# Kernel optimization log

Measured on AMD Instinct MI355X. Metric: run time of the kernel, lower is better.

The kernel has to match this reference:

```python
import jax, jax.numpy as jnp
import numpy as np

B, N = 4096, 2048


def setup_inputs() -> dict:
    key = jax.random.key(0)
    k1, k2, k3, k4 = jax.random.split(key, 4)
    return {
        "src_pts3d": jax.random.normal(k1, (B, N, 3), dtype=jnp.float32),
        "tgt_pts3d": jax.random.normal(k2, (B, N, 3), dtype=jnp.float32),
        "kpt_src_mask": jax.random.uniform(k3, (B, N), dtype=jnp.float32),
        "kpt_tgt_mask": jax.random.uniform(k4, (B, N), dtype=jnp.float32),
    }


def reference(src_pts3d, tgt_pts3d, kpt_src_mask, kpt_tgt_mask):
    # H = src^T @ diag(mask_tgt) @ tgt, fused as a masked row-scale contraction: [B,3,3]
    H = jnp.einsum('bnc,bn,bnd->bcd', src_pts3d, kpt_tgt_mask, tgt_pts3d)
    # torch.svd returns V (H = U S V^T); jnp returns Vh, so V = Vh^T
    u, s, vh = jnp.linalg.svd(H)
    v = jnp.swapaxes(vh, -1, -2)              # [B,3,3]
    ut = jnp.swapaxes(u, -1, -2)              # [B,3,3]
    r = v @ ut
    det = jnp.linalg.det(r)                   # [B]
    # branch-free reflection fix: negate 3rd column of V when det(r) < 0
    sign = jnp.where(det < 0, -1.0, 1.0)
    col_scale = jnp.stack([jnp.ones_like(sign), jnp.ones_like(sign), sign], axis=-1)  # [B,3]
    R = (v * col_scale[:, None, :]) @ ut
    return R
```

## Files before the change

kernel.cpp:

```cpp
#include <hip/hip_runtime.h>
#include <math.h>

#define BATCH 4096
#define NPTS  2048
#define THREADS 256

typedef float f32x4 __attribute__((ext_vector_type(4)));

__device__ __forceinline__ f32x4 ntload(const f32x4* p) {
    return __builtin_nontemporal_load(p);
}

#define ACC(sx, sy, sz, tx, ty, tz, mm) do {                                   \
    float d0 = (mm) * (tx), d1 = (mm) * (ty), d2 = (mm) * (tz);                \
    h[0] = fmaf((sx), d0, h[0]); h[1] = fmaf((sx), d1, h[1]); h[2] = fmaf((sx), d2, h[2]); \
    h[3] = fmaf((sy), d0, h[3]); h[4] = fmaf((sy), d1, h[4]); h[5] = fmaf((sy), d2, h[5]); \
    h[6] = fmaf((sz), d0, h[6]); h[7] = fmaf((sz), d1, h[7]); h[8] = fmaf((sz), d2, h[8]); \
} while (0)

__global__ __launch_bounds__(THREADS, 4)
void reduce_kernel(const float* __restrict__ src, const float* __restrict__ tgt,
                   const float* __restrict__ mask, float* __restrict__ Hout)
{
    const int b   = blockIdx.x;
    const int t   = threadIdx.x;
    const f32x4* s4 = (const f32x4*)(src  + (size_t)b * (NPTS * 3));
    const f32x4* t4 = (const f32x4*)(tgt  + (size_t)b * (NPTS * 3));
    const f32x4* m4 = (const f32x4*)(mask + (size_t)b * NPTS);

    f32x4 m0  = ntload(&m4[t]);
    f32x4 m1  = ntload(&m4[t + 256]);
    f32x4 sa0 = ntload(&s4[3 * t + 0]);
    f32x4 sb0 = ntload(&s4[3 * t + 1]);
    f32x4 sc0 = ntload(&s4[3 * t + 2]);
    f32x4 ta0 = ntload(&t4[3 * t + 0]);
    f32x4 tb0 = ntload(&t4[3 * t + 1]);
    f32x4 tc0 = ntload(&t4[3 * t + 2]);
    f32x4 sa1 = ntload(&s4[3 * (t + 256) + 0]);
    f32x4 sb1 = ntload(&s4[3 * (t + 256) + 1]);
    f32x4 sc1 = ntload(&s4[3 * (t + 256) + 2]);
    f32x4 ta1 = ntload(&t4[3 * (t + 256) + 0]);
    f32x4 tb1 = ntload(&t4[3 * (t + 256) + 1]);
    f32x4 tc1 = ntload(&t4[3 * (t + 256) + 2]);

    float h[9] = {0.f, 0.f, 0.f, 0.f, 0.f, 0.f, 0.f, 0.f, 0.f};
    ACC(sa0.x, sa0.y, sa0.z, ta0.x, ta0.y, ta0.z, m0.x);
    ACC(sa0.w, sb0.x, sb0.y, ta0.w, tb0.x, tb0.y, m0.y);
    ACC(sb0.z, sb0.w, sc0.x, tb0.z, tb0.w, tc0.x, m0.z);
    ACC(sc0.y, sc0.z, sc0.w, tc0.y, tc0.z, tc0.w, m0.w);
    ACC(sa1.x, sa1.y, sa1.z, ta1.x, ta1.y, ta1.z, m1.x);
    ACC(sa1.w, sb1.x, sb1.y, ta1.w, tb1.x, tb1.y, m1.y);
    ACC(sb1.z, sb1.w, sc1.x, tb1.z, tb1.w, tc1.x, m1.z);
    ACC(sc1.y, sc1.z, sc1.w, tc1.y, tc1.z, tc1.w, m1.w);

#pragma unroll
    for (int off = 32; off > 0; off >>= 1) {
#pragma unroll
        for (int i = 0; i < 9; ++i) h[i] += __shfl_down(h[i], off);
    }

    __shared__ float shred[THREADS / 64][9];
    const int wid  = t >> 6;
    const int lane = t & 63;
    if (lane == 0) {
#pragma unroll
        for (int i = 0; i < 9; ++i) shred[wid][i] = h[i];
    }
    __syncthreads();

    if (t < 9) {
        Hout[(size_t)b * 9 + t] =
            shred[0][t] + shred[1][t] + shred[2][t] + shred[3][t];
    }
}

__global__ __launch_bounds__(THREADS)
void solve_kernel(const float* __restrict__ Hin, float* __restrict__ out)
{
    const int b = blockIdx.x * THREADS + threadIdx.x;
    if (b >= BATCH) return;

    double H[3][3];
#pragma unroll
    for (int i = 0; i < 9; ++i)
        H[i / 3][i % 3] = (double)Hin[(size_t)b * 9 + i];

    double A[3][3];
#pragma unroll
    for (int i = 0; i < 3; ++i)
#pragma unroll
        for (int j = 0; j < 3; ++j)
            A[i][j] = H[0][i] * H[0][j] + H[1][i] * H[1][j] + H[2][i] * H[2][j];

    double V[3][3] = {{1, 0, 0}, {0, 1, 0}, {0, 0, 1}};

    const int pq[3][3] = {{0, 1, 2}, {0, 2, 1}, {1, 2, 0}};
    for (int sweep = 0; sweep < 6; ++sweep) {
        for (int r = 0; r < 3; ++r) {
            const int p = pq[r][0], q = pq[r][1], k = pq[r][2];
            double apq = A[p][q];
            if (fabs(apq) > 1e-300) {
                double theta = (A[q][q] - A[p][p]) / (2.0 * apq);
                double t = 1.0 / (fabs(theta) + sqrt(theta * theta + 1.0));
                if (theta < 0.0) t = -t;
                double c = 1.0 / sqrt(t * t + 1.0);
                double s = t * c;
                double app = A[p][p], aqq = A[q][q];
                A[p][p] = app - t * apq;
                A[q][q] = aqq + t * apq;
                A[p][q] = A[q][p] = 0.0;
                double akp = A[k][p], akq = A[k][q];
                A[k][p] = A[p][k] = c * akp - s * akq;
                A[k][q] = A[q][k] = s * akp + c * akq;
#pragma unroll
                for (int i = 0; i < 3; ++i) {
                    double vip = V[i][p], viq = V[i][q];
                    V[i][p] = c * vip - s * viq;
                    V[i][q] = s * vip + c * viq;
                }
            }
        }
    }

    int i0 = 0;
    if (A[1][1] > A[i0][i0]) i0 = 1;
    if (A[2][2] > A[i0][i0]) i0 = 2;
    const int ca = (i0 + 1) % 3, cb = (i0 + 2) % 3;
    const int i1 = (A[ca][ca] >= A[cb][cb]) ? ca : cb;

    double v0[3], v1[3];
#pragma unroll
    for (int i = 0; i < 3; ++i) { v0[i] = V[i][i0]; v1[i] = V[i][i1]; }

    double b0[3], b1[3];
#pragma unroll
    for (int r = 0; r < 3; ++r) {
        b0[r] = H[r][0] * v0[0] + H[r][1] * v0[1] + H[r][2] * v0[2];
        b1[r] = H[r][0] * v1[0] + H[r][1] * v1[1] + H[r][2] * v1[2];
    }
    double n0 = b0[0] * b0[0] + b0[1] * b0[1] + b0[2] * b0[2];
    double inv0 = 1.0 / sqrt(fmax(n0, 1e-300));
    double u0[3] = {b0[0] * inv0, b0[1] * inv0, b0[2] * inv0};
    double d01 = u0[0] * b1[0] + u0[1] * b1[1] + u0[2] * b1[2];
    double w[3] = {b1[0] - d01 * u0[0], b1[1] - d01 * u0[1], b1[2] - d01 * u0[2]};
    double nw = w[0] * w[0] + w[1] * w[1] + w[2] * w[2];
    double inv1 = 1.0 / sqrt(fmax(nw, 1e-300));
    double u1[3] = {w[0] * inv1, w[1] * inv1, w[2] * inv1};
    double u2[3] = {u0[1] * u1[2] - u0[2] * u1[1],
                    u0[2] * u1[0] - u0[0] * u1[2],
                    u0[0] * u1[1] - u0[1] * u1[0]};
    double v2[3] = {v0[1] * v1[2] - v0[2] * v1[1],
                    v0[2] * v1[0] - v0[0] * v1[2],
                    v0[0] * v1[1] - v0[1] * v1[0]};

    float* o = out + (size_t)b * 9;
#pragma unroll
    for (int r = 0; r < 3; ++r)
#pragma unroll
        for (int c = 0; c < 3; ++c)
            o[r * 3 + c] = (float)(v0[r] * u0[c] + v1[r] * u1[c] + v2[r] * u2[c]);
}

extern "C" void kernel_launch(void* const* d_in, const int* in_sizes, int n_in,
                              void* d_out, int out_size, void* d_ws, size_t ws_size,
                              hipStream_t stream) {
    const float* src  = (const float*)d_in[0];
    const float* tgt  = (const float*)d_in[1];
    const float* mask = (const float*)d_in[3];
    float* out = (float*)d_out;
    float* Hws = (float*)d_ws;

    reduce_kernel<<<BATCH, THREADS, 0, stream>>>(src, tgt, mask, Hws);
    solve_kernel<<<(BATCH + THREADS - 1) / THREADS, THREADS, 0, stream>>>(Hws, out);
}
```

Baseline: 251.3 us.

## Fuse reduction and per-batch SVD solve into a single kernel

Merges the reduction kernel and the Jacobi/SVD solve kernel so that thread 0 of each block sums the shared-memory partials and runs the 3x3 solve directly. This removes the second kernel launch and the round trip of H through global workspace. In exchange, the serial double-precision solve now runs on one lane per block at the tail of each block, occupying that block's slot while other lanes idle. The sweep loop is also marked unrolled.

```diff
diff --git a/kernel.cpp b/kernel.cpp
--- a/kernel.cpp
+++ b/kernel.cpp
@@ -19,8 +19,8 @@
 } while (0)
 
 __global__ __launch_bounds__(THREADS, 4)
-void reduce_kernel(const float* __restrict__ src, const float* __restrict__ tgt,
-                   const float* __restrict__ mask, float* __restrict__ Hout)
+void fused_kernel(const float* __restrict__ src, const float* __restrict__ tgt,
+                  const float* __restrict__ mask, float* __restrict__ out)
 {
     const int b   = blockIdx.x;
     const int t   = threadIdx.x;
@@ -68,22 +68,13 @@
     }
     __syncthreads();
 
-    if (t < 9) {
-        Hout[(size_t)b * 9 + t] =
-            shred[0][t] + shred[1][t] + shred[2][t] + shred[3][t];
-    }
-}
-
-__global__ __launch_bounds__(THREADS)
-void solve_kernel(const float* __restrict__ Hin, float* __restrict__ out)
-{
-    const int b = blockIdx.x * THREADS + threadIdx.x;
-    if (b >= BATCH) return;
+    if (t != 0) return;
 
     double H[3][3];
 #pragma unroll
     for (int i = 0; i < 9; ++i)
-        H[i / 3][i % 3] = (double)Hin[(size_t)b * 9 + i];
+        H[i / 3][i % 3] = (double)(shred[0][i] + shred[1][i] +
+                                   shred[2][i] + shred[3][i]);
 
     double A[3][3];
 #pragma unroll
@@ -96,18 +87,19 @@
 
     const int pq[3][3] = {{0, 1, 2}, {0, 2, 1}, {1, 2, 0}};
     for (int sweep = 0; sweep < 6; ++sweep) {
+#pragma unroll
         for (int r = 0; r < 3; ++r) {
             const int p = pq[r][0], q = pq[r][1], k = pq[r][2];
             double apq = A[p][q];
             if (fabs(apq) > 1e-300) {
                 double theta = (A[q][q] - A[p][p]) / (2.0 * apq);
-                double t = 1.0 / (fabs(theta) + sqrt(theta * theta + 1.0));
-                if (theta < 0.0) t = -t;
-                double c = 1.0 / sqrt(t * t + 1.0);
-                double s = t * c;
+                double tt = 1.0 / (fabs(theta) + sqrt(theta * theta + 1.0));
+                if (theta < 0.0) tt = -tt;
+                double c = 1.0 / sqrt(tt * tt + 1.0);
+                double s = tt * c;
                 double app = A[p][p], aqq = A[q][q];
-                A[p][p] = app - t * apq;
-                A[q][q] = aqq + t * apq;
+                A[p][p] = app - tt * apq;
+                A[q][q] = aqq + tt * apq;
                 A[p][q] = A[q][p] = 0.0;
                 double akp = A[k][p], akq = A[k][q];
                 A[k][p] = A[p][k] = c * akp - s * akq;
@@ -149,16 +141,16 @@
     double u2[3] = {u0[1] * u1[2] - u0[2] * u1[1],
                     u0[2] * u1[0] - u0[0] * u1[2],
                     u0[0] * u1[1] - u0[1] * u1[0]};
-    double v2[3] = {v0[1] * v1[2] - v0[2] * v1[1],
-                    v0[2] * v1[0] - v0[0] * v1[2],
-                    v0[0] * v1[1] - v0[1] * v1[0]};
+    double vc2[3] = {v0[1] * v1[2] - v0[2] * v1[1],
+                     v0[2] * v1[0] - v0[0] * v1[2],
+                     v0[0] * v1[1] - v0[1] * v1[0]};
 
     float* o = out + (size_t)b * 9;
 #pragma unroll
     for (int r = 0; r < 3; ++r)
 #pragma unroll
         for (int c = 0; c < 3; ++c)
-            o[r * 3 + c] = (float)(v0[r] * u0[c] + v1[r] * u1[c] + v2[r] * u2[c]);
+            o[r * 3 + c] = (float)(v0[r] * u0[c] + v1[r] * u1[c] + vc2[r] * u2[c]);
 }
 
 extern "C" void kernel_launch(void* const* d_in, const int* in_sizes, int n_in,
@@ -168,8 +160,6 @@
     const float* tgt  = (const float*)d_in[1];
     const float* mask = (const float*)d_in[3];
     float* out = (float*)d_out;
-    float* Hws = (float*)d_ws;
 
-    reduce_kernel<<<BATCH, THREADS, 0, stream>>>(src, tgt, mask, Hws);
-    solve_kernel<<<(BATCH + THREADS - 1) / THREADS, THREADS, 0, stream>>>(Hws, out);
+    fused_kernel<<<BATCH, THREADS, 0, stream>>>(src, tgt, mask, out);
 }
```

Result: slower. 267.0 us (+6.3%).
